# Performance work log

Measured on AMD Instinct MI355X. Metric: run time of the kernel, lower is better.

## Reference

```python
import jax, jax.numpy as jnp
import numpy as np

B, S, E, H, D = 4, 2048, 1024, 16, 64   # batch, seq, embed, heads, head_dim
NUM_BUCKETS, MAX_DISTANCE = 32, 128


def _relative_position_bucket(relative_position, num_buckets, max_distance):
    # causal T5-style bucketing
    max_exact = num_buckets // 2
    max_distance = max(max_distance, max_exact + 1)
    distance = jnp.maximum(-relative_position, 0)
    is_small = distance < max_exact
    safe_distance = jnp.maximum(distance, 1)
    log_scale = jnp.log(safe_distance / max_exact) / jnp.log(max_distance / max_exact)
    large_bucket = max_exact + (log_scale * (num_buckets - max_exact)).astype(jnp.int32)
    large_bucket = jnp.minimum(large_bucket, num_buckets - 1)
    return jnp.where(is_small, distance, large_bucket)


def setup_inputs() -> dict:
    key = jax.random.key(0)
    ks = jax.random.split(key, 7)
    w_scale = 1.0 / np.sqrt(E)
    inputs_q = jax.random.normal(ks[0], (B, S, E), jnp.float32)
    inputs_kv = jax.random.normal(ks[1], (B, S, E), jnp.float32)
    Wq = jax.random.normal(ks[2], (E, H * D), jnp.float32) * w_scale
    Wk = jax.random.normal(ks[3], (E, H * D), jnp.float32) * w_scale
    Wv = jax.random.normal(ks[4], (E, H * D), jnp.float32) * w_scale
    Wo = jax.random.normal(ks[5], (H * D, E), jnp.float32) * (1.0 / np.sqrt(H * D))
    rel_bias = jax.random.normal(ks[6], (H, NUM_BUCKETS), jnp.float32) * 0.02
    mask = jnp.tril(jnp.ones((S, S), dtype=bool))[None, None]  # [1,1,Q,K] causal
    return {"inputs_q": inputs_q, "inputs_kv": inputs_kv, "mask": mask,
            "Wq": Wq, "Wk": Wk, "Wv": Wv, "Wo": Wo, "rel_bias": rel_bias}


def reference(inputs_q, inputs_kv, mask, Wq, Wk, Wv, Wo, rel_bias):
    batch, q_len, embed = inputs_q.shape
    k_len = inputs_kv.shape[1]
    q = (inputs_q @ Wq).reshape(batch, q_len, H, D)
    k = (inputs_kv @ Wk).reshape(batch, k_len, H, D)
    v = (inputs_kv @ Wv).reshape(batch, k_len, H, D)
    attention = jnp.einsum("bqhd,bkhd->bhqk", q, k) * (1.0 / jnp.sqrt(D))
    # T5 relative position bias
    rel_pos = jnp.arange(k_len, dtype=jnp.int32)[None, :] - jnp.arange(q_len, dtype=jnp.int32)[:, None]
    bucket = _relative_position_bucket(rel_pos, NUM_BUCKETS, MAX_DISTANCE)  # [Q,K]
    attention = attention + jnp.take(rel_bias, bucket, axis=1)[None]  # [1,H,Q,K]
    attention = jnp.where(mask, attention, jnp.finfo(jnp.float32).min)
    normalized = jax.nn.softmax(attention, axis=-1)
    output = jnp.einsum("bhqk,bkhd->bqhd", normalized, v).reshape(batch, q_len, H * D)
    return output @ Wo
```

## Files before the change

### kernel.cpp

```cpp
#include <hip/hip_runtime.h>

typedef unsigned short u16;
typedef unsigned int u32;
typedef __bf16 bf16x8 __attribute__((ext_vector_type(8)));
typedef float f32x2 __attribute__((ext_vector_type(2)));
typedef float f32x4 __attribute__((ext_vector_type(4)));
typedef float f32x16 __attribute__((ext_vector_type(16)));

#define S_LEN 2048
#define EMB 1024
#define NH 16
#define HD 64
#define LOG2E 1.44269504088896f
#define QSCALE (0.125f * LOG2E)
#define THRL 11.5415603f
#define FB(r) ((((r) ^ ((r) >> 2))) & 3)

__device__ __forceinline__ u16 f2bf(float f) {
  union { float f; unsigned u; } v; v.f = f;
  unsigned r = (v.u + 0x7fffu + ((v.u >> 16) & 1u)) >> 16;
  return (u16)r;
}

__device__ __forceinline__ u32 packbf(float a, float b) {
  union { __bf16 h[2]; u32 u; } x;
  x.h[0] = (__bf16)a; x.h[1] = (__bf16)b;
  return x.u;
}

__device__ __forceinline__ void g2l16(const void* g, void* l) {
  __builtin_amdgcn_global_load_lds(
      (const unsigned int __attribute__((address_space(1)))*)g,
      (unsigned int __attribute__((address_space(3)))*)l, 16, 0, 0);
}

__device__ __forceinline__ float permswap_max(float a) {
  auto r = __builtin_amdgcn_permlane32_swap(__float_as_int(a), __float_as_int(a), false, false);
  return fmaxf(__int_as_float(r[0]), __int_as_float(r[1]));
}
__device__ __forceinline__ float permswap_add(float a) {
  auto r = __builtin_amdgcn_permlane32_swap(__float_as_int(a), __float_as_int(a), false, false);
  return __int_as_float(r[0]) + __int_as_float(r[1]);
}


__global__ void cvt_bf16(const float* __restrict__ src, u16* __restrict__ dst, int n4) {
  int i = blockIdx.x * blockDim.x + threadIdx.x;
  if (i < n4) {
    float4 f = ((const float4*)src)[i];
    ushort4 o;
    o.x = f2bf(f.x); o.y = f2bf(f.y); o.z = f2bf(f.z); o.w = f2bf(f.w);
    ((ushort4*)dst)[i] = o;
  }
}

__global__ void transcvt(const float* __restrict__ W, u16* __restrict__ Wt) {
  __shared__ float t[32][33];
  int k0 = blockIdx.x * 32, n0 = blockIdx.y * 32;
  int tx = threadIdx.x & 31, ty = threadIdx.x >> 5;
#pragma unroll
  for (int i = 0; i < 4; i++) t[ty + i * 8][tx] = W[(k0 + ty + i * 8) * 1024 + n0 + tx];
  __syncthreads();
#pragma unroll
  for (int i = 0; i < 4; i++) Wt[(n0 + ty + i * 8) * 1024 + k0 + tx] = f2bf(t[tx][ty + i * 8]);
}

__global__ void build_bias(const float* __restrict__ rel, float* __restrict__ tbl) {
  int i = blockIdx.x * 256 + threadIdx.x;
  int h = i >> 11, dist = i & 2047;
  int bk;
  if (dist < 16) {
    bk = dist;
  } else {
    float ls = logf((float)dist * (1.0f / 16.0f)) * (1.0f / logf(8.0f));
    bk = 16 + (int)(ls * 16.0f);
    if (bk > 31) bk = 31;
  }
  tbl[i] = rel[h * 32 + bk] * LOG2E;
}


__global__ __launch_bounds__(256, 4) void gemm_qkv(const u16* __restrict__ Aq,
                                                   const u16* __restrict__ Akv,
                                                   const u16* __restrict__ Wt,
                                                   u16* __restrict__ QKV, float qscale) {
  constexpr int K = EMB;
  __shared__ u16 As[128 * 32];
  __shared__ u16 Bs[128 * 32];

  const int bid = blockIdx.x;
  const int xcd = bid & 7, idx = bid >> 3;
  const int mt = xcd * 8 + (idx & 7);
  const int nt = idx >> 3;
  const int m0 = mt * 128;
  const int n0 = nt * 128;
  const int mat = n0 >> 10;
  const u16* A = (mat == 0) ? Aq : Akv;

  const int tid = threadIdx.x;
  const int lane = tid & 63;
  const int wid = tid >> 6;
  const int wm = (wid >> 1) * 64;
  const int wn = (wid & 1) * 64;
  const int la = lane & 15;
  const int lg = lane >> 4;

  const int r0 = tid >> 2;
  const int c0 = ((tid & 3) ^ FB(r0)) * 8;
  const u16* gA = A + (size_t)(m0 + r0) * K + c0;
  const u16* gB = Wt + (size_t)(n0 + r0) * K + c0;
  u16* lA = As + tid * 8;
  u16* lB = Bs + tid * 8;

  f32x4 acc[4][4] = {};

  for (int k0 = 0; k0 < K; k0 += 32) {
    g2l16(gA, lA);
    g2l16(gA + 64 * K, lA + 2048);
    g2l16(gB, lB);
    g2l16(gB + 64 * K, lB + 2048);
    gA += 32;
    gB += 32;
    __syncthreads();
    bf16x8 af[4], bb[4];
#pragma unroll
    for (int mf = 0; mf < 4; mf++) {
      int row = wm + mf * 16 + la;
      af[mf] = *(const bf16x8*)&As[row * 32 + ((lg ^ FB(row)) << 3)];
    }
#pragma unroll
    for (int nf = 0; nf < 4; nf++) {
      int row = wn + nf * 16 + la;
      bb[nf] = *(const bf16x8*)&Bs[row * 32 + ((lg ^ FB(row)) << 3)];
    }
#pragma unroll
    for (int mf = 0; mf < 4; mf++)
#pragma unroll
      for (int nf = 0; nf < 4; nf++)
        acc[mf][nf] =
            __builtin_amdgcn_mfma_f32_16x16x32_bf16(af[mf], bb[nf], acc[mf][nf], 0, 0, 0);
    __syncthreads();
  }

  const float sc = (mat == 0) ? qscale : 1.0f;
#pragma unroll
  for (int mf = 0; mf < 4; mf++)
#pragma unroll
    for (int nf = 0; nf < 4; nf++)
#pragma unroll
      for (int r = 0; r < 4; r++) {
        int m = m0 + wm + mf * 16 + lg * 4 + r;
        int n = n0 + wn + nf * 16 + la;
        float v = acc[mf][nf][r] * sc;
        int b = m >> 11, s = m & 2047, h = (n >> 6) & 15, d = n & 63;
        size_t base = (size_t)mat << 23;
        if (mat < 2)
          QKV[base + (((size_t)(b * 16 + h) * 2048 + s) << 6) + d] = f2bf(v);
        else
          QKV[base + (((size_t)(b * 16 + h) * 64 + d) << 11) + s] = f2bf(v);
      }
}


__global__ __launch_bounds__(256, 4) void gemm_out(const u16* __restrict__ A,
                                                   const u16* __restrict__ Bt,
                                                   float* __restrict__ C) {
  constexpr int K = EMB;
  __shared__ u16 As[128 * 32];
  __shared__ u16 Bs[128 * 32];
  const int bid = blockIdx.x;
  const int xcd = bid & 7, idx = bid >> 3;
  const int mt = xcd * 8 + (idx & 7);
  const int nt = idx >> 3;
  const int m0 = mt * 128;
  const int n0 = nt * 128;
  const int tid = threadIdx.x;
  const int lane = tid & 63;
  const int wid = tid >> 6;
  const int wm = (wid >> 1) * 64;
  const int wn = (wid & 1) * 64;
  const int la = lane & 15;
  const int lg = lane >> 4;

  const int r0 = tid >> 2;
  const int c0 = ((tid & 3) ^ FB(r0)) * 8;
  const u16* gA = A + (size_t)(m0 + r0) * K + c0;
  const u16* gB = Bt + (size_t)(n0 + r0) * K + c0;

  f32x4 acc[4][4] = {};

  for (int k0 = 0; k0 < K; k0 += 32) {
    g2l16(gA, As + tid * 8);
    g2l16(gA + 64 * K, As + tid * 8 + 2048);
    g2l16(gB, Bs + tid * 8);
    g2l16(gB + 64 * K, Bs + tid * 8 + 2048);
    gA += 32;
    gB += 32;
    __syncthreads();
    bf16x8 af[4], bb[4];
#pragma unroll
    for (int mf = 0; mf < 4; mf++) {
      int row = wm + mf * 16 + la;
      af[mf] = *(const bf16x8*)&As[row * 32 + ((lg ^ FB(row)) << 3)];
    }
#pragma unroll
    for (int nf = 0; nf < 4; nf++) {
      int row = wn + nf * 16 + la;
      bb[nf] = *(const bf16x8*)&Bs[row * 32 + ((lg ^ FB(row)) << 3)];
    }
#pragma unroll
    for (int mf = 0; mf < 4; mf++)
#pragma unroll
      for (int nf = 0; nf < 4; nf++)
        acc[mf][nf] =
            __builtin_amdgcn_mfma_f32_16x16x32_bf16(af[mf], bb[nf], acc[mf][nf], 0, 0, 0);
    __syncthreads();
  }

#pragma unroll
  for (int mf = 0; mf < 4; mf++)
#pragma unroll
    for (int nf = 0; nf < 4; nf++)
#pragma unroll
      for (int r = 0; r < 4; r++) {
        int m = m0 + wm + mf * 16 + lg * 4 + r;
        int n = n0 + wn + nf * 16 + la;
        C[(size_t)m * 1024 + n] = acc[mf][nf][r];
      }
}


__device__ __forceinline__ void softmax_repack(const f32x16* sacc, int kv0, int qw, int q, int hi,
                                               const float* bias_s, float bias31, float& mrun,
                                               float& lrun, f32x16& o0, f32x16& o1,
                                               u32 (&paw)[4][4]) {
  f32x2 pf[16];
  float adde = 0.f;
  if (kv0 + 176 <= qw) {
#pragma unroll
    for (int j = 0; j < 16; j++) {
      const int nf = j >> 3, r = (j & 7) * 2;
      pf[j] = (f32x2){sacc[nf][r], sacc[nf][r + 1]};
    }
    adde = bias31;
  } else {
    const int qb2 = q - kv0 - 4 * hi;
    const float* bp = bias_s + (qb2 - 59);
    if (kv0 + 63 <= qw) {
#pragma unroll
      for (int j = 0; j < 16; j++) {
        const int nf = j >> 3, r = (j & 7) * 2;
        const int Cn = nf * 32 + (r & 3) + ((r >> 2) << 3);
        f32x2 bv = {bp[59 - Cn], bp[58 - Cn]};
        pf[j] = (f32x2){sacc[nf][r], sacc[nf][r + 1]} + bv;
      }
    } else {
#pragma unroll
      for (int j = 0; j < 16; j++) {
        const int nf = j >> 3, r = (j & 7) * 2;
        const int Cn = nf * 32 + (r & 3) + ((r >> 2) << 3);
        pf[j].x = (Cn <= qb2) ? (sacc[nf][r] + bp[59 - Cn]) : -1e30f;
        pf[j].y = (Cn + 1 <= qb2) ? (sacc[nf][r + 1] + bp[58 - Cn]) : -1e30f;
      }
    }
  }

  f32x2 t8[8];
#pragma unroll
  for (int i = 0; i < 8; i++) t8[i] = __builtin_elementwise_max(pf[i], pf[i + 8]);
#pragma unroll
  for (int i = 0; i < 4; i++) t8[i] = __builtin_elementwise_max(t8[i], t8[i + 4]);
  f32x2 m2 = __builtin_elementwise_max(__builtin_elementwise_max(t8[0], t8[1]),
                                       __builtin_elementwise_max(t8[2], t8[3]));
  float mt = fmaxf(m2.x, m2.y) + adde;
  mt = permswap_max(mt);

  if (__any(mt > mrun + THRL)) {
    float mn = fmaxf(mrun, mt);
    float s = exp2f(mrun - mn);
    mrun = mn;
    lrun *= s;
    o0 *= s;
    o1 *= s;
  }
  const f32x2 ec2 = {adde - mrun, adde - mrun};

  f32x2 s8[8];
#pragma unroll
  for (int j = 0; j < 16; j++) {
    f32x2 a = pf[j] + ec2;
    f32x2 p = {exp2f(a.x), exp2f(a.y)};
    pf[j] = p;
    if (j < 8) s8[j] = p;
    else s8[j - 8] += p;
  }
#pragma unroll
  for (int i = 0; i < 4; i++) s8[i] += s8[i + 4];
  f32x2 s2 = (s8[0] + s8[1]) + (s8[2] + s8[3]);
  lrun += permswap_add(s2.x + s2.y);

#pragma unroll
  for (int ks = 0; ks < 4; ks++) {
    const int j0b = (ks >> 1) * 8 + (ks & 1) * 4;
#pragma unroll
    for (int half = 0; half < 2; half++) {
      u32 Y0 = packbf(pf[j0b + half].x, pf[j0b + half].y);
      u32 Y1 = packbf(pf[j0b + 2 + half].x, pf[j0b + 2 + half].y);
      auto r = __builtin_amdgcn_permlane32_swap((int)Y0, (int)Y1, false, false);
      paw[ks][half] = (u32)r[0];
      paw[ks][2 + half] = (u32)r[1];
    }
  }
}

template <int CUR>
__device__ __forceinline__ void tile_body(int t, int ntblk, int qmax, int qw, int q, int hi,
                                          int la, int tid, const u16*& kp, const u16*& vp,
                                          u16 (*Ks)[64 * 64], u16 (*Vs)[64 * 64],
                                          const bf16x8 (&qfrag)[4], const float* bias_s,
                                          float bias31, float& mrun, float& lrun, f32x16& o0,
                                          f32x16& o1) {
  if (t + 1 < ntblk) {
    u16* lK = Ks[CUR ^ 1] + tid * 8;
    u16* lV = Vs[CUR ^ 1] + tid * 8;
    g2l16(kp, lK);
    g2l16(kp + 32 * 64, lK + 2048);
    g2l16(vp, lV);
    g2l16(vp + 32 * S_LEN, lV + 2048);
    kp += 4096;
    vp += 64;
    asm volatile("s_waitcnt vmcnt(4)" ::: "memory");
  } else {
    asm volatile("s_waitcnt vmcnt(0)" ::: "memory");
  }
  __builtin_amdgcn_s_barrier();
  asm volatile("" ::: "memory");

  const int kv0 = t << 6;
  if (kv0 <= qmax) {
    f32x16 sacc[2] = {};
    __builtin_amdgcn_s_setprio(1);
#pragma unroll
    for (int kk = 0; kk < 4; kk++)
#pragma unroll
      for (int nf = 0; nf < 2; nf++) {
        int row = nf * 32 + la;
        bf16x8 kf = *(const bf16x8*)&Ks[CUR][row * 64 + (((kk * 2 + hi) ^ (row & 7)) << 3)];
        sacc[nf] = __builtin_amdgcn_mfma_f32_32x32x16_bf16(kf, qfrag[kk], sacc[nf], 0, 0, 0);
      }
    __builtin_amdgcn_s_setprio(0);

    u32 paw[4][4];
    softmax_repack(sacc, kv0, qw, q, hi, bias_s, bias31, mrun, lrun, o0, o1, paw);

    __builtin_amdgcn_s_setprio(1);
#pragma unroll
    for (int d2 = 0; d2 < 2; d2++) {
      f32x16& oa = d2 ? o1 : o0;
#pragma unroll
      for (int ks = 0; ks < 4; ks++) {
        int row = d2 * 32 + la;
        bf16x8 vf = *(const bf16x8*)&Vs[CUR][row * 64 + (((ks * 2 + hi) ^ (row & 7)) << 3)];
        union { u32 w[4]; bf16x8 v; } pu;
        pu.w[0] = paw[ks][0]; pu.w[1] = paw[ks][1];
        pu.w[2] = paw[ks][2]; pu.w[3] = paw[ks][3];
        oa = __builtin_amdgcn_mfma_f32_32x32x16_bf16(vf, pu.v, oa, 0, 0, 0);
      }
    }
    __builtin_amdgcn_s_setprio(0);
  }

  asm volatile("" ::: "memory");
  __builtin_amdgcn_s_barrier();
  asm volatile("" ::: "memory");
}

__global__ __launch_bounds__(256, 3) void attn_kernel(const u16* __restrict__ Qb,
                                                      const u16* __restrict__ Kb,
                                                      const u16* __restrict__ Vtb,
                                                      const float* __restrict__ btbl,
                                                      u16* __restrict__ O) {
  __shared__ u16 Ks[2][64 * 64];
  __shared__ u16 Vs[2][64 * 64];
  __shared__ float bias_s[S_LEN];

  const int bh = blockIdx.x;
  const int h = bh & (NH - 1);
  const int b = bh >> 4;
  const int qt = 15 - blockIdx.y;
  const int q0 = qt * 128;
  const int tid = threadIdx.x;
  const int lane = tid & 63;
  const int w = tid >> 6;
  const int la = lane & 31;
  const int hi = lane >> 5;

  {
    const float4* src = (const float4*)(btbl + h * S_LEN);
    float4* dst = (float4*)bias_s;
    dst[tid] = src[tid];
    dst[tid + 256] = src[tid + 256];
  }

  const u16* Qg = Qb + (size_t)bh * S_LEN * HD;
  const u16* Kg = Kb + (size_t)bh * S_LEN * HD;
  const u16* Vg = Vtb + (size_t)bh * HD * S_LEN;

  const int qw = q0 + w * 32;
  const int q = qw + la;

  bf16x8 qfrag[4];
#pragma unroll
  for (int kk = 0; kk < 4; kk++)
    qfrag[kk] = *(const bf16x8*)&Qg[(size_t)q * HD + kk * 16 + hi * 8];

  f32x16 o0 = {}, o1 = {};
  float mrun = -1e30f;
  float lrun = 0.f;

  const int sr = tid >> 3;
  const int scz = ((tid & 7) ^ (sr & 7)) * 8;
  const u16* kp = Kg + sr * 64 + scz;
  const u16* vp = Vg + (size_t)sr * S_LEN + scz;

  const int ntblk = (q0 + 128) >> 6;
  const int qmax = qw + 31;

  g2l16(kp, Ks[0] + tid * 8);
  g2l16(kp + 32 * 64, Ks[0] + tid * 8 + 2048);
  g2l16(vp, Vs[0] + tid * 8);
  g2l16(vp + 32 * S_LEN, Vs[0] + tid * 8 + 2048);
  kp += 4096;
  vp += 64;
  asm volatile("s_waitcnt lgkmcnt(0)" ::: "memory");
  __builtin_amdgcn_s_barrier();
  asm volatile("" ::: "memory");

  const float bias31 = bias_s[S_LEN - 1];

  int t = 0;
  while (t < ntblk) {
    tile_body<0>(t, ntblk, qmax, qw, q, hi, la, tid, kp, vp, Ks, Vs, qfrag, bias_s, bias31,
                 mrun, lrun, o0, o1);
    ++t;
    tile_body<1>(t, ntblk, qmax, qw, q, hi, la, tid, kp, vp, Ks, Vs, qfrag, bias_s, bias31,
                 mrun, lrun, o0, o1);
    ++t;
  }

  const float inv = 1.0f / lrun;
  u16* Og = O + ((size_t)(b * S_LEN + q)) * EMB + h * HD;
#pragma unroll
  for (int d2 = 0; d2 < 2; d2++) {
    const f32x16& oa = d2 ? o1 : o0;
#pragma unroll
    for (int g = 0; g < 4; g++) {
      ushort4 ov;
      ov.x = f2bf(oa[g * 4 + 0] * inv);
      ov.y = f2bf(oa[g * 4 + 1] * inv);
      ov.z = f2bf(oa[g * 4 + 2] * inv);
      ov.w = f2bf(oa[g * 4 + 3] * inv);
      *(ushort4*)&Og[d2 * 32 + g * 8 + hi * 4] = ov;
    }
  }
}


extern "C" void kernel_launch(void* const* d_in, const int* in_sizes, int n_in, void* d_out,
                              int out_size, void* d_ws, size_t ws_size, hipStream_t stream) {
  (void)in_sizes; (void)n_in; (void)out_size; (void)ws_size;
  const float* inq = (const float*)d_in[0];
  const float* inkv = (const float*)d_in[1];
  const float* Wq = (const float*)d_in[3];
  const float* Wk = (const float*)d_in[4];
  const float* Wv = (const float*)d_in[5];
  const float* Wo = (const float*)d_in[6];
  const float* rel = (const float*)d_in[7];
  float* out = (float*)d_out;

  char* ws = (char*)d_ws;
  size_t off = 0;
  auto alloc = [&](size_t bytes) {
    void* p = ws + off;
    off += (bytes + 255) & ~(size_t)255;
    return p;
  };
  u16* Aq = (u16*)alloc(16777216);
  u16* Akv = (u16*)alloc(16777216);
  u16* Wqkvt = (u16*)alloc(6291456);
  u16* Wot = (u16*)alloc(2097152);
  u16* QKV = (u16*)alloc(50331648);
  u16* Ob = (u16*)alloc(16777216);
  float* btbl = (float*)alloc(131072);

  u16* Qb = QKV;
  u16* Kb = QKV + 8388608;
  u16* Vtb = QKV + 16777216;

  cvt_bf16<<<8192, 256, 0, stream>>>(inq, Aq, 2097152);
  cvt_bf16<<<8192, 256, 0, stream>>>(inkv, Akv, 2097152);
  transcvt<<<dim3(32, 32), 256, 0, stream>>>(Wq, Wqkvt);
  transcvt<<<dim3(32, 32), 256, 0, stream>>>(Wk, Wqkvt + 1048576);
  transcvt<<<dim3(32, 32), 256, 0, stream>>>(Wv, Wqkvt + 2097152);
  transcvt<<<dim3(32, 32), 256, 0, stream>>>(Wo, Wot);
  build_bias<<<128, 256, 0, stream>>>(rel, btbl);

  gemm_qkv<<<1536, 256, 0, stream>>>(Aq, Akv, Wqkvt, QKV, QSCALE);
  attn_kernel<<<dim3(64, 16), 256, 0, stream>>>(Qb, Kb, Vtb, btbl, Ob);
  gemm_out<<<512, 256, 0, stream>>>(Ob, Wot, out);
}
```

Measured before the change: 217.5 us.

## Double-buffer GEMM LDS tiles, merge prep kernels, restructure attention barriers

The QKV and output GEMMs now keep two LDS buffers for A and B. The next k-tile is prefetched while MFMAs run on the current one, and the MFMA block is given raised wave priority. The six conversion and transpose launches are merged into two kernels to cut launch overhead. The attention tile loop drops its mid-tile vmcnt wait and barrier and instead uses one end-of-phase wait that drains all loads. That removes the partial overlap the attention loop previously had, and the doubled LDS use in the GEMMs may reduce occupancy.

```diff
diff --git a/kernel.cpp b/kernel.cpp
--- a/kernel.cpp
+++ b/kernel.cpp
@@ -43,19 +43,38 @@
   return __int_as_float(r[0]) + __int_as_float(r[1]);
 }
 
-
-__global__ void cvt_bf16(const float* __restrict__ src, u16* __restrict__ dst, int n4) {
+__device__ __forceinline__ void phase_end() {
+  asm volatile("s_waitcnt lgkmcnt(0)" ::: "memory");
+  asm volatile("s_waitcnt vmcnt(0)" ::: "memory");
+  __builtin_amdgcn_s_barrier();
+  asm volatile("" ::: "memory");
+}
+
+
+__global__ void cvt_bf16_2(const float* __restrict__ aq, const float* __restrict__ akv,
+                           u16* __restrict__ dq, u16* __restrict__ dkv) {
   int i = blockIdx.x * blockDim.x + threadIdx.x;
-  if (i < n4) {
-    float4 f = ((const float4*)src)[i];
-    ushort4 o;
-    o.x = f2bf(f.x); o.y = f2bf(f.y); o.z = f2bf(f.z); o.w = f2bf(f.w);
-    ((ushort4*)dst)[i] = o;
-  }
-}
-
-__global__ void transcvt(const float* __restrict__ W, u16* __restrict__ Wt) {
+  const float4* s;
+  ushort4* d;
+  int j;
+  if (i < 2097152) {
+    s = (const float4*)aq; d = (ushort4*)dq; j = i;
+  } else {
+    s = (const float4*)akv; d = (ushort4*)dkv; j = i - 2097152;
+  }
+  float4 f = s[j];
+  ushort4 o;
+  o.x = f2bf(f.x); o.y = f2bf(f.y); o.z = f2bf(f.z); o.w = f2bf(f.w);
+  d[j] = o;
+}
+
+__global__ void transcvt4(const float* __restrict__ W0, const float* __restrict__ W1,
+                          const float* __restrict__ W2, const float* __restrict__ W3,
+                          u16* __restrict__ Dqkv, u16* __restrict__ Do) {
   __shared__ float t[32][33];
+  const int z = blockIdx.z;
+  const float* W = (z == 0) ? W0 : (z == 1) ? W1 : (z == 2) ? W2 : W3;
+  u16* Wt = (z < 3) ? (Dqkv + (size_t)z * 1048576) : Do;
   int k0 = blockIdx.x * 32, n0 = blockIdx.y * 32;
   int tx = threadIdx.x & 31, ty = threadIdx.x >> 5;
 #pragma unroll
@@ -85,8 +104,8 @@
                                                    const u16* __restrict__ Wt,
                                                    u16* __restrict__ QKV, float qscale) {
   constexpr int K = EMB;
-  __shared__ u16 As[128 * 32];
-  __shared__ u16 Bs[128 * 32];
+  __shared__ u16 As[2][128 * 32];
+  __shared__ u16 Bs[2][128 * 32];
 
   const int bid = blockIdx.x;
   const int xcd = bid & 7, idx = bid >> 3;
@@ -109,37 +128,53 @@
   const int c0 = ((tid & 3) ^ FB(r0)) * 8;
   const u16* gA = A + (size_t)(m0 + r0) * K + c0;
   const u16* gB = Wt + (size_t)(n0 + r0) * K + c0;
-  u16* lA = As + tid * 8;
-  u16* lB = Bs + tid * 8;
 
   f32x4 acc[4][4] = {};
 
-  for (int k0 = 0; k0 < K; k0 += 32) {
-    g2l16(gA, lA);
-    g2l16(gA + 64 * K, lA + 2048);
-    g2l16(gB, lB);
-    g2l16(gB + 64 * K, lB + 2048);
-    gA += 32;
-    gB += 32;
-    __syncthreads();
+  g2l16(gA, As[0] + tid * 8);
+  g2l16(gA + 64 * K, As[0] + tid * 8 + 2048);
+  g2l16(gB, Bs[0] + tid * 8);
+  g2l16(gB + 64 * K, Bs[0] + tid * 8 + 2048);
+  gA += 32;
+  gB += 32;
+  asm volatile("s_waitcnt vmcnt(0)" ::: "memory");
+  __builtin_amdgcn_s_barrier();
+  asm volatile("" ::: "memory");
+
+  for (int t = 0; t < 32; ++t) {
+    const int cur = t & 1;
+    if (t < 31) {
+      u16* lA = As[cur ^ 1] + tid * 8;
+      u16* lB = Bs[cur ^ 1] + tid * 8;
+      g2l16(gA, lA);
+      g2l16(gA + 64 * K, lA + 2048);
+      g2l16(gB, lB);
+      g2l16(gB + 64 * K, lB + 2048);
+      gA += 32;
+      gB += 32;
+    }
+
     bf16x8 af[4], bb[4];
 #pragma unroll
     for (int mf = 0; mf < 4; mf++) {
       int row = wm + mf * 16 + la;
-      af[mf] = *(const bf16x8*)&As[row * 32 + ((lg ^ FB(row)) << 3)];
+      af[mf] = *(const bf16x8*)&As[cur][row * 32 + ((lg ^ FB(row)) << 3)];
     }
 #pragma unroll
     for (int nf = 0; nf < 4; nf++) {
       int row = wn + nf * 16 + la;
-      bb[nf] = *(const bf16x8*)&Bs[row * 32 + ((lg ^ FB(row)) << 3)];
-    }
+      bb[nf] = *(const bf16x8*)&Bs[cur][row * 32 + ((lg ^ FB(row)) << 3)];
+    }
+    __builtin_amdgcn_s_setprio(1);
 #pragma unroll
     for (int mf = 0; mf < 4; mf++)
 #pragma unroll
       for (int nf = 0; nf < 4; nf++)
         acc[mf][nf] =
             __builtin_amdgcn_mfma_f32_16x16x32_bf16(af[mf], bb[nf], acc[mf][nf], 0, 0, 0);
-    __syncthreads();
+    __builtin_amdgcn_s_setprio(0);
+
+    phase_end();
   }
 
   const float sc = (mat == 0) ? qscale : 1.0f;
@@ -166,8 +201,8 @@
                                                    const u16* __restrict__ Bt,
                                                    float* __restrict__ C) {
   constexpr int K = EMB;
-  __shared__ u16 As[128 * 32];
-  __shared__ u16 Bs[128 * 32];
+  __shared__ u16 As[2][128 * 32];
+  __shared__ u16 Bs[2][128 * 32];
   const int bid = blockIdx.x;
   const int xcd = bid & 7, idx = bid >> 3;
   const int mt = xcd * 8 + (idx & 7);
@@ -189,32 +224,50 @@
 
   f32x4 acc[4][4] = {};
 
-  for (int k0 = 0; k0 < K; k0 += 32) {
-    g2l16(gA, As + tid * 8);
-    g2l16(gA + 64 * K, As + tid * 8 + 2048);
-    g2l16(gB, Bs + tid * 8);
-    g2l16(gB + 64 * K, Bs + tid * 8 + 2048);
-    gA += 32;
-    gB += 32;
-    __syncthreads();
+  g2l16(gA, As[0] + tid * 8);
+  g2l16(gA + 64 * K, As[0] + tid * 8 + 2048);
+  g2l16(gB, Bs[0] + tid * 8);
+  g2l16(gB + 64 * K, Bs[0] + tid * 8 + 2048);
+  gA += 32;
+  gB += 32;
+  asm volatile("s_waitcnt vmcnt(0)" ::: "memory");
+  __builtin_amdgcn_s_barrier();
+  asm volatile("" ::: "memory");
+
+  for (int t = 0; t < 32; ++t) {
+    const int cur = t & 1;
+    if (t < 31) {
+      u16* lA = As[cur ^ 1] + tid * 8;
+      u16* lB = Bs[cur ^ 1] + tid * 8;
+      g2l16(gA, lA);
+      g2l16(gA + 64 * K, lA + 2048);
+      g2l16(gB, lB);
+      g2l16(gB + 64 * K, lB + 2048);
+      gA += 32;
+      gB += 32;
+    }
+
     bf16x8 af[4], bb[4];
 #pragma unroll
     for (int mf = 0; mf < 4; mf++) {
       int row = wm + mf * 16 + la;
-      af[mf] = *(const bf16x8*)&As[row * 32 + ((lg ^ FB(row)) << 3)];
+      af[mf] = *(const bf16x8*)&As[cur][row * 32 + ((lg ^ FB(row)) << 3)];
     }
 #pragma unroll
     for (int nf = 0; nf < 4; nf++) {
       int row = wn + nf * 16 + la;
-      bb[nf] = *(const bf16x8*)&Bs[row * 32 + ((lg ^ FB(row)) << 3)];
-    }
+      bb[nf] = *(const bf16x8*)&Bs[cur][row * 32 + ((lg ^ FB(row)) << 3)];
+    }
+    __builtin_amdgcn_s_setprio(1);
 #pragma unroll
     for (int mf = 0; mf < 4; mf++)
 #pragma unroll
       for (int nf = 0; nf < 4; nf++)
         acc[mf][nf] =
             __builtin_amdgcn_mfma_f32_16x16x32_bf16(af[mf], bb[nf], acc[mf][nf], 0, 0, 0);
-    __syncthreads();
+    __builtin_amdgcn_s_setprio(0);
+
+    phase_end();
   }
 
 #pragma unroll
@@ -329,12 +382,7 @@
     g2l16(vp + 32 * S_LEN, lV + 2048);
     kp += 4096;
     vp += 64;
-    asm volatile("s_waitcnt vmcnt(4)" ::: "memory");
-  } else {
-    asm volatile("s_waitcnt vmcnt(0)" ::: "memory");
-  }
-  __builtin_amdgcn_s_barrier();
-  asm volatile("" ::: "memory");
+  }
 
   const int kv0 = t << 6;
   if (kv0 <= qmax) {
@@ -370,9 +418,7 @@
     __builtin_amdgcn_s_setprio(0);
   }
 
-  asm volatile("" ::: "memory");
-  __builtin_amdgcn_s_barrier();
-  asm volatile("" ::: "memory");
+  phase_end();
 }
 
 __global__ __launch_bounds__(256, 3) void attn_kernel(const u16* __restrict__ Qb,
@@ -432,9 +478,7 @@
   g2l16(vp + 32 * S_LEN, Vs[0] + tid * 8 + 2048);
   kp += 4096;
   vp += 64;
-  asm volatile("s_waitcnt lgkmcnt(0)" ::: "memory");
-  __builtin_amdgcn_s_barrier();
-  asm volatile("" ::: "memory");
+  phase_end();
 
   const float bias31 = bias_s[S_LEN - 1];
 
@@ -497,12 +541,8 @@
   u16* Kb = QKV + 8388608;
   u16* Vtb = QKV + 16777216;
 
-  cvt_bf16<<<8192, 256, 0, stream>>>(inq, Aq, 2097152);
-  cvt_bf16<<<8192, 256, 0, stream>>>(inkv, Akv, 2097152);
-  transcvt<<<dim3(32, 32), 256, 0, stream>>>(Wq, Wqkvt);
-  transcvt<<<dim3(32, 32), 256, 0, stream>>>(Wk, Wqkvt + 1048576);
-  transcvt<<<dim3(32, 32), 256, 0, stream>>>(Wv, Wqkvt + 2097152);
-  transcvt<<<dim3(32, 32), 256, 0, stream>>>(Wo, Wot);
+  cvt_bf16_2<<<16384, 256, 0, stream>>>(inq, inkv, Aq, Akv);
+  transcvt4<<<dim3(32, 32, 4), 256, 0, stream>>>(Wq, Wk, Wv, Wo, Wqkvt, Wot);
   build_bias<<<128, 256, 0, stream>>>(rel, btbl);
 
   gemm_qkv<<<1536, 256, 0, stream>>>(Aq, Akv, Wqkvt, QKV, QSCALE);
```

Result: no change. 214.8 us (-1.3%).
